# Kernel tuning notes

Measured on AMD Instinct MI355X. Metric: run time of the kernel, lower is better.

Reference implementation:

```python
import jax, jax.numpy as jnp
import numpy as np

ND = 64       # dijetFeatures (channels)
NPAIR = 6     # six dijet slots


def _interleave(x, d):
    # x: [n, nd, 12] -> [n, nd, 6, 2]; d: [n, nd, 6] -> [n, nd, 6, 1]
    n, nd, _ = x.shape
    xr = x.reshape(n, nd, NPAIR, 2)
    z = jnp.concatenate([xr, d[..., None]], axis=-1)  # [n, nd, 6, 3]
    return z


def _conv_s3(z, W, b):
    # z: [n, in, 6, 3] grouped windows; W: [out, in, 3]; stride-3 k-3 conv == per-window contraction
    return jnp.einsum('bisk,oik->bos', z, W) + b[None, :, None]  # [n, out, 6]


def setup_inputs() -> dict:
    key = jax.random.key(0)
    ks = jax.random.split(key, 8)
    n = 65536
    inp = {
        'x': jax.random.normal(ks[0], (n, ND, 12), dtype=jnp.float32),
        'd': jax.random.normal(ks[1], (n, ND, NPAIR), dtype=jnp.float32),
        'W1': jax.random.normal(ks[2], (ND, ND, 3), dtype=jnp.float32) * 0.05,
        'b1': jax.random.normal(ks[3], (ND,), dtype=jnp.float32) * 0.05,
        'W2': jax.random.normal(ks[4], (ND, ND, 3), dtype=jnp.float32) * 0.05,
        'b2': jax.random.normal(ks[5], (ND,), dtype=jnp.float32) * 0.05,
        'W3': jax.random.normal(ks[6], (ND, ND, 3), dtype=jnp.float32) * 0.05,
        'b3': jax.random.normal(ks[7], (ND,), dtype=jnp.float32) * 0.05,
    }
    return inp


def reference(x, d, W1, b1, W2, b2, W3, b3):
    d1 = d
    d = jax.nn.relu(_conv_s3(_interleave(x, d), W1, b1))
    d = jax.nn.relu(_conv_s3(_interleave(x, d), W2, b2))
    d = _conv_s3(_interleave(x, d), W3, b3)
    return jax.nn.relu(d + d1)
```

## Files before the change

### kernel.cpp

```cpp
#include <hip/hip_runtime.h>

#define ND 64
#define NPAIR 6

typedef short bf16x8 __attribute__((ext_vector_type(8)));
typedef float floatx4 __attribute__((ext_vector_type(4)));

static constexpr int SPB  = 16;
static constexpr int ROWS = SPB * NPAIR;
static constexpr int ASTR = 200;
static constexpr int DSTR = 72;

__device__ __forceinline__ unsigned short f2bf(float f) {
    unsigned u = __builtin_bit_cast(unsigned, f);
    u += 0x7FFFu + ((u >> 16) & 1u);
    return (unsigned short)(u >> 16);
}
__device__ __forceinline__ unsigned f2bf2(float lo, float hi) {
    return (unsigned)f2bf(lo) | ((unsigned)f2bf(hi) << 16);
}
__device__ __forceinline__ float bf2f(unsigned short h) {
    unsigned u = ((unsigned)h) << 16;
    return __builtin_bit_cast(float, u);
}

__global__ void repack_w(const float* __restrict__ W1, const float* __restrict__ W2,
                         const float* __restrict__ W3, unsigned short* __restrict__ P) {
    int idx = blockIdx.x * 256 + threadIdx.x;
    if (idx >= 3 * 64 * 192) return;
    int j = idx % 192;
    int n = (idx / 192) % 64;
    int L = idx / (192 * 64);
    const float* W = (L == 0) ? W1 : (L == 1) ? W2 : W3;
    float v = (j < 128) ? W[n * 192 + (j >> 1) * 3 + (j & 1)]
                        : W[n * 192 + (j - 128) * 3 + 2];
    P[idx] = f2bf(v);
}

__global__ __launch_bounds__(256, 3) void dijet_main(
    const float* __restrict__ x, const float* __restrict__ d,
    const float* __restrict__ b1, const float* __restrict__ b2,
    const float* __restrict__ b3, const unsigned short* __restrict__ Wp,
    float* __restrict__ out)
{
    __shared__ unsigned short A[ROWS * ASTR];
    __shared__ unsigned short D0[ROWS * DSTR];

    const int t  = threadIdx.x;
    const int b0 = blockIdx.x * SPB;

    {
        const float4* x4 = (const float4*)(x + (size_t)b0 * (ND * 12));
        unsigned* A32 = (unsigned*)A;
        #pragma unroll
        for (int m = 0; m < 12; ++m) {
            int idx = m * 256 + t;
            float4 v = x4[idx];
            int b   = idx / 192;
            int rem = idx - b * 192;
            int i   = rem / 3;
            int c0  = (rem - i * 3) * 4;
            int row0 = b * 6 + (c0 >> 1);
            A32[row0 * (ASTR / 2) + i]       = f2bf2(v.x, v.y);
            A32[(row0 + 1) * (ASTR / 2) + i] = f2bf2(v.z, v.w);
        }
    }
    {
        const float2* d2 = (const float2*)(d + (size_t)b0 * (ND * NPAIR));
        #pragma unroll
        for (int m = 0; m < 12; ++m) {
            int idx = m * 256 + t;
            float2 v = d2[idx];
            int e   = idx * 2;
            int b   = e / 384;
            int rem = e - b * 384;
            int i   = rem / 6;
            int s   = rem - i * 6;
            int row = b * 6 + s;
            unsigned short lo = f2bf(v.x), hi = f2bf(v.y);
            A[row * ASTR + 128 + i]       = lo;
            A[(row + 1) * ASTR + 128 + i] = hi;
            D0[row * DSTR + i]            = lo;
            D0[(row + 1) * DSTR + i]      = hi;
        }
    }
    __syncthreads();

    const int wave = t >> 6;
    const int lane = t & 63;
    const int mhalf = wave & 1;
    const int nhalf = wave >> 1;
    const int l15  = lane & 15;
    const int quad = lane >> 4;

    const int mbase = mhalf * 48;
    const int nbase = nhalf * 32;

    #pragma unroll
    for (int L = 0; L < 3; ++L) {
        const float* bL = (L == 0) ? b1 : (L == 1) ? b2 : b3;
        const unsigned short* WL = Wp + L * (64 * 192);

        bf16x8 Bf[2][6];
        #pragma unroll
        for (int nt = 0; nt < 2; ++nt)
            #pragma unroll
            for (int kk = 0; kk < 6; ++kk)
                Bf[nt][kk] = *(const bf16x8*)(WL + (nbase + nt * 16 + l15) * 192 + kk * 32 + quad * 8);
        float bias0 = bL[nbase + l15];
        float bias1 = bL[nbase + 16 + l15];

        floatx4 acc[3][2] = {};
        #pragma unroll
        for (int kk = 0; kk < 6; ++kk) {
            #pragma unroll
            for (int mt = 0; mt < 3; ++mt) {
                bf16x8 Af = *(const bf16x8*)(A + (mbase + mt * 16 + l15) * ASTR + kk * 32 + quad * 8);
                acc[mt][0] = __builtin_amdgcn_mfma_f32_16x16x32_bf16(Af, Bf[0][kk], acc[mt][0], 0, 0, 0);
                acc[mt][1] = __builtin_amdgcn_mfma_f32_16x16x32_bf16(Af, Bf[1][kk], acc[mt][1], 0, 0, 0);
            }
        }

        if (L < 2) {
            __syncthreads();
            #pragma unroll
            for (int mt = 0; mt < 3; ++mt) {
                #pragma unroll
                for (int nt = 0; nt < 2; ++nt) {
                    float bias = nt ? bias1 : bias0;
                    int o = nbase + nt * 16 + l15;
                    #pragma unroll
                    for (int r = 0; r < 4; ++r) {
                        int row = mbase + mt * 16 + quad * 4 + r;
                        float v = acc[mt][nt][r] + bias;
                        v = v > 0.f ? v : 0.f;
                        A[row * ASTR + 128 + o] = f2bf(v);
                    }
                }
            }
            __syncthreads();
        } else {
            #pragma unroll
            for (int mt = 0; mt < 3; ++mt) {
                #pragma unroll
                for (int nt = 0; nt < 2; ++nt) {
                    float bias = nt ? bias1 : bias0;
                    int o = nbase + nt * 16 + l15;
                    #pragma unroll
                    for (int r = 0; r < 4; ++r) {
                        int row = mbase + mt * 16 + quad * 4 + r;
                        float v = acc[mt][nt][r] + bias + bf2f(D0[row * DSTR + o]);
                        v = v > 0.f ? v : 0.f;
                        int bl = row / 6;
                        int s  = row - bl * 6;
                        out[(size_t)(b0 + bl) * (ND * NPAIR) + o * 6 + s] = v;
                    }
                }
            }
        }
    }
}

extern "C" void kernel_launch(void* const* d_in, const int* in_sizes, int n_in,
                              void* d_out, int out_size, void* d_ws, size_t ws_size,
                              hipStream_t stream)
{
    const float* x  = (const float*)d_in[0];
    const float* dd = (const float*)d_in[1];
    const float* W1 = (const float*)d_in[2];
    const float* b1 = (const float*)d_in[3];
    const float* W2 = (const float*)d_in[4];
    const float* b2 = (const float*)d_in[5];
    const float* W3 = (const float*)d_in[6];
    const float* b3 = (const float*)d_in[7];
    float* out = (float*)d_out;
    unsigned short* Wp = (unsigned short*)d_ws;

    int n = in_sizes[0] / (ND * 12);

    repack_w<<<144, 256, 0, stream>>>(W1, W2, W3, Wp);
    dijet_main<<<n / SPB, 256, 0, stream>>>(x, dd, b1, b2, b3, Wp, out);
}
```

Measured before the change: 443.8 us.

## Stage final output in LDS for coalesced stores and fp32 residual from global

Removes the separate D0 bf16 residual buffer and, in the last layer, writes the pre-activation result into shared memory in output layout. It then reads it back as float4, adds the fp32 residual re-read from global d, applies relu, and stores coalesced float4 to out. Global loads in the prologue are batched six at a time to raise memory-level parallelism, and launch bounds move from 3 to 4 blocks per CU using the freed LDS. The cost is an extra read of d and additional barriers, in exchange for replacing scattered strided output stores with coalesced ones. The residual now uses the exact fp32 d instead of a bf16-rounded copy.

Measured after the change: 421.7 us. 1.05x faster.

```diff
diff --git a/kernel.cpp b/kernel.cpp
--- a/kernel.cpp
+++ b/kernel.cpp
@@ -9,7 +9,6 @@
 static constexpr int SPB  = 16;
 static constexpr int ROWS = SPB * NPAIR;
 static constexpr int ASTR = 200;
-static constexpr int DSTR = 72;
 
 __device__ __forceinline__ unsigned short f2bf(float f) {
     unsigned u = __builtin_bit_cast(unsigned, f);
@@ -18,10 +17,6 @@
 }
 __device__ __forceinline__ unsigned f2bf2(float lo, float hi) {
     return (unsigned)f2bf(lo) | ((unsigned)f2bf(hi) << 16);
-}
-__device__ __forceinline__ float bf2f(unsigned short h) {
-    unsigned u = ((unsigned)h) << 16;
-    return __builtin_bit_cast(float, u);
 }
 
 __global__ void repack_w(const float* __restrict__ W1, const float* __restrict__ W2,
@@ -37,14 +32,14 @@
     P[idx] = f2bf(v);
 }
 
-__global__ __launch_bounds__(256, 3) void dijet_main(
+__global__ __launch_bounds__(256, 4) void dijet_main(
     const float* __restrict__ x, const float* __restrict__ d,
     const float* __restrict__ b1, const float* __restrict__ b2,
     const float* __restrict__ b3, const unsigned short* __restrict__ Wp,
     float* __restrict__ out)
 {
-    __shared__ unsigned short A[ROWS * ASTR];
-    __shared__ unsigned short D0[ROWS * DSTR];
+    __shared__ __align__(16) unsigned short A[ROWS * ASTR];
+    float* Ct = (float*)A;
 
     const int t  = threadIdx.x;
     const int b0 = blockIdx.x * SPB;
@@ -53,35 +48,42 @@
         const float4* x4 = (const float4*)(x + (size_t)b0 * (ND * 12));
         unsigned* A32 = (unsigned*)A;
         #pragma unroll
-        for (int m = 0; m < 12; ++m) {
-            int idx = m * 256 + t;
-            float4 v = x4[idx];
-            int b   = idx / 192;
-            int rem = idx - b * 192;
-            int i   = rem / 3;
-            int c0  = (rem - i * 3) * 4;
-            int row0 = b * 6 + (c0 >> 1);
-            A32[row0 * (ASTR / 2) + i]       = f2bf2(v.x, v.y);
-            A32[(row0 + 1) * (ASTR / 2) + i] = f2bf2(v.z, v.w);
+        for (int half = 0; half < 2; ++half) {
+            float4 v[6];
+            #pragma unroll
+            for (int m = 0; m < 6; ++m) v[m] = x4[(half * 6 + m) * 256 + t];
+            #pragma unroll
+            for (int m = 0; m < 6; ++m) {
+                int idx = (half * 6 + m) * 256 + t;
+                int b   = idx / 192;
+                int rem = idx - b * 192;
+                int i   = rem / 3;
+                int c0  = (rem - i * 3) * 4;
+                int row0 = b * 6 + (c0 >> 1);
+                A32[row0 * (ASTR / 2) + i]       = f2bf2(v[m].x, v[m].y);
+                A32[(row0 + 1) * (ASTR / 2) + i] = f2bf2(v[m].z, v[m].w);
+            }
         }
     }
     {
         const float2* d2 = (const float2*)(d + (size_t)b0 * (ND * NPAIR));
         #pragma unroll
-        for (int m = 0; m < 12; ++m) {
-            int idx = m * 256 + t;
-            float2 v = d2[idx];
-            int e   = idx * 2;
-            int b   = e / 384;
-            int rem = e - b * 384;
-            int i   = rem / 6;
-            int s   = rem - i * 6;
-            int row = b * 6 + s;
-            unsigned short lo = f2bf(v.x), hi = f2bf(v.y);
-            A[row * ASTR + 128 + i]       = lo;
-            A[(row + 1) * ASTR + 128 + i] = hi;
-            D0[row * DSTR + i]            = lo;
-            D0[(row + 1) * DSTR + i]      = hi;
+        for (int half = 0; half < 2; ++half) {
+            float2 v[6];
+            #pragma unroll
+            for (int m = 0; m < 6; ++m) v[m] = d2[(half * 6 + m) * 256 + t];
+            #pragma unroll
+            for (int m = 0; m < 6; ++m) {
+                int idx = (half * 6 + m) * 256 + t;
+                int e   = idx * 2;
+                int b   = e / 384;
+                int rem = e - b * 384;
+                int i   = rem / 6;
+                int s   = rem - i * 6;
+                int row = b * 6 + s;
+                A[row * ASTR + 128 + i]       = f2bf(v[m].x);
+                A[(row + 1) * ASTR + 128 + i] = f2bf(v[m].y);
+            }
         }
     }
     __syncthreads();
@@ -140,6 +142,7 @@
             }
             __syncthreads();
         } else {
+            __syncthreads();
             #pragma unroll
             for (int mt = 0; mt < 3; ++mt) {
                 #pragma unroll
@@ -149,13 +152,27 @@
                     #pragma unroll
                     for (int r = 0; r < 4; ++r) {
                         int row = mbase + mt * 16 + quad * 4 + r;
-                        float v = acc[mt][nt][r] + bias + bf2f(D0[row * DSTR + o]);
-                        v = v > 0.f ? v : 0.f;
-                        int bl = row / 6;
-                        int s  = row - bl * 6;
-                        out[(size_t)(b0 + bl) * (ND * NPAIR) + o * 6 + s] = v;
+                        int bl  = row / 6;
+                        int s   = row - bl * 6;
+                        Ct[bl * (ND * NPAIR) + o * NPAIR + s] = acc[mt][nt][r] + bias;
                     }
                 }
+            }
+            __syncthreads();
+            const float4* dres4 = (const float4*)(d + (size_t)b0 * (ND * NPAIR));
+            float4*       out4  = (float4*)(out + (size_t)b0 * (ND * NPAIR));
+            const float4* Ct4   = (const float4*)Ct;
+            #pragma unroll
+            for (int m = 0; m < 6; ++m) {
+                int idx = m * 256 + t;
+                float4 c = Ct4[idx];
+                float4 dv = dres4[idx];
+                float4 r;
+                r.x = c.x + dv.x; r.x = r.x > 0.f ? r.x : 0.f;
+                r.y = c.y + dv.y; r.y = r.y > 0.f ? r.y : 0.f;
+                r.z = c.z + dv.z; r.z = r.z > 0.f ? r.z : 0.f;
+                r.w = c.w + dv.w; r.w = r.w > 0.f ? r.w : 0.f;
+                out4[idx] = r;
             }
         }
     }
```
